# Kernel optimization log

Measured on AMD Instinct MI355X. Metric: run time of the kernel, lower is better.

Reference implementation:

```python
import jax, jax.numpy as jnp
import numpy as np

B, P, E, D, A, M, V, L = 128, 196, 2048, 512, 512, 512, 10000, 21


def setup_inputs() -> dict:
    key = jax.random.key(0)
    ks = jax.random.split(key, 24)
    s = 0.02
    encoder_out = jax.random.normal(ks[0], (B, P, E), jnp.float32)
    encoded_captions = jax.random.randint(ks[1], (B, L), 0, V)
    caption_lengths = jax.random.randint(ks[2], (B,), 2, L + 1).at[0].set(L)
    return {
        "encoder_out": encoder_out,
        "encoded_captions": encoded_captions,
        "caption_lengths": caption_lengths,
        "emb_table": jax.random.normal(ks[3], (V, M), jnp.float32) * s,
        "enc_att_w": jax.random.normal(ks[4], (E, A), jnp.float32) * s,
        "enc_att_b": jnp.zeros((A,), jnp.float32),
        "dec_att_w": jax.random.normal(ks[5], (D, A), jnp.float32) * s,
        "dec_att_b": jnp.zeros((A,), jnp.float32),
        "full_att_w": jax.random.normal(ks[6], (A,), jnp.float32) * s,
        "full_att_b": jnp.zeros((), jnp.float32),
        "init_h_w": jax.random.normal(ks[7], (E, D), jnp.float32) * s,
        "init_h_b": jnp.zeros((D,), jnp.float32),
        "init_c_w": jax.random.normal(ks[8], (E, D), jnp.float32) * s,
        "init_c_b": jnp.zeros((D,), jnp.float32),
        "f_beta_w": jax.random.normal(ks[9], (D, E), jnp.float32) * s,
        "f_beta_b": jnp.zeros((E,), jnp.float32),
        "lstm_w_ih": jax.random.normal(ks[10], (4 * D, M + E), jnp.float32) * s,
        "lstm_b_ih": jnp.zeros((4 * D,), jnp.float32),
        "lstm_w_hh": jax.random.normal(ks[11], (4 * D, D), jnp.float32) * s,
        "lstm_b_hh": jnp.zeros((4 * D,), jnp.float32),
        "fc_w": jax.random.normal(ks[12], (V, D), jnp.float32) * s,
        "fc_b": jnp.zeros((V,), jnp.float32),
    }


def reference(encoder_out, encoded_captions, caption_lengths, emb_table,
              enc_att_w, enc_att_b, dec_att_w, dec_att_b, full_att_w, full_att_b,
              init_h_w, init_h_b, init_c_w, init_c_b, f_beta_w, f_beta_b,
              lstm_w_ih, lstm_b_ih, lstm_w_hh, lstm_b_hh, fc_w, fc_b):
    # sort by caption length descending (as in torch)
    order = jnp.argsort(-caption_lengths)
    enc = encoder_out[order]                 # [B,P,E]
    caps = encoded_captions[order]           # [B,L]
    dec_len = caption_lengths[order] - 1     # [B]
    T = caps.shape[1] - 1

    emb_seq = emb_table[caps]                # [B,L,M]
    mean = enc.mean(axis=1)                  # [B,E]
    h0 = mean @ init_h_w + init_h_b
    c0 = mean @ init_c_w + init_c_b
    att1 = enc @ enc_att_w + enc_att_b       # [B,P,A] (hoisted: constant over t)

    def step(carry, t):
        h, c = carry
        att2 = h @ dec_att_w + dec_att_b                              # [B,A]
        e = jnp.einsum('bpa,a->bp', jax.nn.relu(att1 + att2[:, None, :]), full_att_w) + full_att_b
        alpha = jax.nn.softmax(e, axis=1)                             # [B,P]
        awe = jnp.einsum('bpe,bp->be', enc, alpha)                    # [B,E]
        gate = jax.nn.sigmoid(h @ f_beta_w + f_beta_b)                # [B,E]
        x = jnp.concatenate([emb_seq[:, t, :], gate * awe], axis=1)   # [B,M+E]
        g = x @ lstm_w_ih.T + lstm_b_ih + h @ lstm_w_hh.T + lstm_b_hh
        i, f, gg, o = jnp.split(g, 4, axis=1)
        c_new = jax.nn.sigmoid(f) * c + jax.nn.sigmoid(i) * jnp.tanh(gg)
        h_new = jax.nn.sigmoid(o) * jnp.tanh(c_new)
        pred = h_new @ fc_w.T + fc_b                                  # [B,V]
        active = (t < dec_len)[:, None]
        pred = jnp.where(active, pred, 0.0)
        alpha = jnp.where(active, alpha, 0.0)
        return (h_new, c_new), (pred, alpha)

    _, (preds, alphas) = jax.lax.scan(step, (h0, c0), jnp.arange(T))
    predictions = jnp.moveaxis(preds, 0, 1)   # [B,T,V]
    alphas = jnp.moveaxis(alphas, 0, 1)       # [B,T,P]
    return predictions, alphas
```

## Files before the change

### kernel.cpp

```cpp
#include <hip/hip_runtime.h>
#include <math.h>

#define B_ 128
#define P_ 196
#define E_ 2048
#define D_ 512
#define A_ 512
#define M_ 512
#define V_ 10000
#define L_ 21
#define T_ 20

__global__ void order_kernel(const int* __restrict__ lens, const int* __restrict__ caps,
                             int* __restrict__ order, int* __restrict__ declen,
                             int* __restrict__ row_map, int* __restrict__ tok_rows) {
  __shared__ int s_order[B_];
  int tid = threadIdx.x;
  if (tid < B_) {
    int li = lens[tid];
    int r = 0;
    for (int j = 0; j < B_; ++j) {
      int lj = lens[j];
      r += (lj > li) || (lj == li && j < tid);
    }
    s_order[r] = tid;
    declen[r] = li - 1;
  }
  __syncthreads();
  if (tid < B_) order[tid] = s_order[tid];
  for (int m = tid; m < B_ * P_; m += blockDim.x) {
    int b = m / P_, p = m - b * P_;
    row_map[m] = s_order[b] * P_ + p;
  }
  for (int i = tid; i < T_ * B_; i += blockDim.x) {
    int t = i >> 7, b = i & 127;
    tok_rows[i] = caps[s_order[b] * L_ + t];
  }
}

__global__ void mean_kernel(const float* __restrict__ enc, const int* __restrict__ order,
                            float* __restrict__ mean) {
  int b = blockIdx.y;
  int e = blockIdx.x * blockDim.x + threadIdx.x;
  int ob = order[b];
  const float* base = enc + (long long)ob * P_ * E_ + e;
  float s = 0.f;
  for (int p = 0; p < P_; ++p) s += base[(long long)p * E_];
  mean[b * E_ + e] = s * (1.0f / P_);
}

template <bool BT, int ACT, int CMAP>
__global__ __launch_bounds__(256) void gemm_kernel(
    const float* __restrict__ A, const float* __restrict__ Bm,
    const float* __restrict__ bias, const float* __restrict__ bias2,
    float* __restrict__ C, int M, int N, int K, int bs,
    const int* __restrict__ row_map, long long c_rstride,
    float* __restrict__ xh_dup, const int* __restrict__ declen) {
  __shared__ float As[16][64];
  __shared__ float Bs[16][64];
  const int tid = threadIdx.x;
  const int bm = blockIdx.y * 64, bn = blockIdx.x * 64;
  const int tm = tid >> 4, tn = tid & 15;

  float acc[4][4];
#pragma unroll
  for (int i = 0; i < 4; ++i)
#pragma unroll
    for (int j = 0; j < 4; ++j) acc[i][j] = 0.f;

  const int lm = tid >> 2;
  const int lk = (tid & 3) * 4;

  for (int k0 = 0; k0 < K; k0 += 16) {
    {
      int m = bm + lm;
      float4 v = make_float4(0.f, 0.f, 0.f, 0.f);
      if (m < M) {
        int row = row_map ? row_map[m] : m;
        v = *(const float4*)(A + (long long)row * K + k0 + lk);
      }
      As[lk + 0][lm] = v.x;
      As[lk + 1][lm] = v.y;
      As[lk + 2][lm] = v.z;
      As[lk + 3][lm] = v.w;
    }
    if (!BT) {
      int k = tid >> 4;
      int n4 = (tid & 15) * 4;
      int n = bn + n4;
      float4 v = make_float4(0.f, 0.f, 0.f, 0.f);
      if (n < N) v = *(const float4*)(Bm + (long long)(k0 + k) * bs + n);
      Bs[k][n4 + 0] = v.x;
      Bs[k][n4 + 1] = v.y;
      Bs[k][n4 + 2] = v.z;
      Bs[k][n4 + 3] = v.w;
    } else {
      int n = bn + lm;
      float4 v = make_float4(0.f, 0.f, 0.f, 0.f);
      if (n < N) v = *(const float4*)(Bm + (long long)n * bs + k0 + lk);
      Bs[lk + 0][lm] = v.x;
      Bs[lk + 1][lm] = v.y;
      Bs[lk + 2][lm] = v.z;
      Bs[lk + 3][lm] = v.w;
    }
    __syncthreads();
#pragma unroll
    for (int k = 0; k < 16; ++k) {
      float a0 = As[k][tm * 4 + 0];
      float a1 = As[k][tm * 4 + 1];
      float a2 = As[k][tm * 4 + 2];
      float a3 = As[k][tm * 4 + 3];
      float b0 = Bs[k][tn * 4 + 0];
      float b1 = Bs[k][tn * 4 + 1];
      float b2 = Bs[k][tn * 4 + 2];
      float b3 = Bs[k][tn * 4 + 3];
      acc[0][0] += a0 * b0; acc[0][1] += a0 * b1; acc[0][2] += a0 * b2; acc[0][3] += a0 * b3;
      acc[1][0] += a1 * b0; acc[1][1] += a1 * b1; acc[1][2] += a1 * b2; acc[1][3] += a1 * b3;
      acc[2][0] += a2 * b0; acc[2][1] += a2 * b1; acc[2][2] += a2 * b2; acc[2][3] += a2 * b3;
      acc[3][0] += a3 * b0; acc[3][1] += a3 * b1; acc[3][2] += a3 * b2; acc[3][3] += a3 * b3;
    }
    __syncthreads();
  }

#pragma unroll
  for (int i = 0; i < 4; ++i) {
    int m = bm + tm * 4 + i;
    if (m >= M) continue;
#pragma unroll
    for (int j = 0; j < 4; ++j) {
      int n = bn + tn * 4 + j;
      if (n >= N) continue;
      float v = acc[i][j];
      if (bias) v += bias[n];
      if (bias2) v += bias2[n];
      if (ACT == 1) v = 1.f / (1.f + __expf(-v));
      if (CMAP == 0) {
        C[(long long)m * c_rstride + n] = v;
        if (xh_dup) xh_dup[m * 2560 + 2048 + n] = v;
      } else {
        int b = m & 127, t = m >> 7;
        bool active = t < declen[b];
        C[(long long)b * (T_ * V_) + (long long)t * V_ + n] = active ? v : 0.f;
      }
    }
  }
}

__global__ __launch_bounds__(256) void step1_kernel(
    const float* __restrict__ h, const float* __restrict__ dec_att_w,
    const float* __restrict__ dec_att_b, const float* __restrict__ f_beta_w,
    const float* __restrict__ f_beta_b, float* __restrict__ att2,
    float* __restrict__ gate) {
  __shared__ float As[16][64];
  __shared__ float Bs[16][64];
  const int tid = threadIdx.x;
  const int bm = blockIdx.y * 64, bn = blockIdx.x * 64;
  const bool isatt = bn < 512;
  const float* Bp = isatt ? dec_att_w : f_beta_w;
  const int bstride = isatt ? 512 : 2048;
  const int ncol0 = isatt ? bn : bn - 512;
  const int tm = tid >> 4, tn = tid & 15;
  float acc[4][4];
#pragma unroll
  for (int i = 0; i < 4; ++i)
#pragma unroll
    for (int j = 0; j < 4; ++j) acc[i][j] = 0.f;
  const int lm = tid >> 2;
  const int lk = (tid & 3) * 4;
  for (int k0 = 0; k0 < 512; k0 += 16) {
    {
      int m = bm + lm;
      float4 v = *(const float4*)(h + m * 512 + k0 + lk);
      As[lk + 0][lm] = v.x;
      As[lk + 1][lm] = v.y;
      As[lk + 2][lm] = v.z;
      As[lk + 3][lm] = v.w;
    }
    {
      int k = tid >> 4;
      int n4 = (tid & 15) * 4;
      float4 v = *(const float4*)(Bp + (k0 + k) * bstride + ncol0 + n4);
      Bs[k][n4 + 0] = v.x;
      Bs[k][n4 + 1] = v.y;
      Bs[k][n4 + 2] = v.z;
      Bs[k][n4 + 3] = v.w;
    }
    __syncthreads();
#pragma unroll
    for (int k = 0; k < 16; ++k) {
      float a0 = As[k][tm * 4 + 0];
      float a1 = As[k][tm * 4 + 1];
      float a2 = As[k][tm * 4 + 2];
      float a3 = As[k][tm * 4 + 3];
      float b0 = Bs[k][tn * 4 + 0];
      float b1 = Bs[k][tn * 4 + 1];
      float b2 = Bs[k][tn * 4 + 2];
      float b3 = Bs[k][tn * 4 + 3];
      acc[0][0] += a0 * b0; acc[0][1] += a0 * b1; acc[0][2] += a0 * b2; acc[0][3] += a0 * b3;
      acc[1][0] += a1 * b0; acc[1][1] += a1 * b1; acc[1][2] += a1 * b2; acc[1][3] += a1 * b3;
      acc[2][0] += a2 * b0; acc[2][1] += a2 * b1; acc[2][2] += a2 * b2; acc[2][3] += a2 * b3;
      acc[3][0] += a3 * b0; acc[3][1] += a3 * b1; acc[3][2] += a3 * b2; acc[3][3] += a3 * b3;
    }
    __syncthreads();
  }
#pragma unroll
  for (int i = 0; i < 4; ++i) {
    int m = bm + tm * 4 + i;
#pragma unroll
    for (int j = 0; j < 4; ++j) {
      int nc = ncol0 + tn * 4 + j;
      float v = acc[i][j];
      if (isatt) {
        att2[m * 512 + nc] = v + dec_att_b[nc];
      } else {
        v += f_beta_b[nc];
        gate[m * 2048 + nc] = 1.f / (1.f + __expf(-v));
      }
    }
  }
}

__global__ __launch_bounds__(256) void esm_kernel(
    const float* __restrict__ att1, const float* __restrict__ att2,
    const float* __restrict__ w, const float* __restrict__ fb,
    const int* __restrict__ declen, int t,
    float* __restrict__ alpha_ws, float* __restrict__ alpha_out) {
  __shared__ float att2_s[A_];
  __shared__ float w_s[A_];
  __shared__ float e_s[P_];
  __shared__ float red[8];
  int b = blockIdx.x, tid = threadIdx.x;
  for (int i = tid; i < A_; i += 256) {
    att2_s[i] = att2[b * A_ + i];
    w_s[i] = w[i];
  }
  __syncthreads();
  int wave = tid >> 6, lane = tid & 63;
  for (int p = wave; p < P_; p += 4) {
    const float* row = att1 + ((long long)b * P_ + p) * A_;
    float s = 0.f;
#pragma unroll
    for (int i = 0; i < A_ / 64; ++i) {
      int idx = lane + i * 64;
      float v = row[idx] + att2_s[idx];
      s += (v > 0.f ? v : 0.f) * w_s[idx];
    }
    for (int off = 32; off; off >>= 1) s += __shfl_down(s, off);
    if (lane == 0) e_s[p] = s + fb[0];
  }
  __syncthreads();
  float m = -1e30f;
  for (int p = tid; p < P_; p += 256) m = fmaxf(m, e_s[p]);
  for (int off = 32; off; off >>= 1) m = fmaxf(m, __shfl_down(m, off));
  if (lane == 0) red[wave] = m;
  __syncthreads();
  m = fmaxf(fmaxf(red[0], red[1]), fmaxf(red[2], red[3]));
  float ssum = 0.f;
  for (int p = tid; p < P_; p += 256) {
    float ev = __expf(e_s[p] - m);
    e_s[p] = ev;
    ssum += ev;
  }
  for (int off = 32; off; off >>= 1) ssum += __shfl_down(ssum, off);
  if (lane == 0) red[4 + wave] = ssum;
  __syncthreads();
  ssum = red[4] + red[5] + red[6] + red[7];
  float inv = 1.f / ssum;
  bool active = (t < declen[b]);
  for (int p = tid; p < P_; p += 256) {
    float al = e_s[p] * inv;
    alpha_ws[b * P_ + p] = al;
    alpha_out[(long long)b * (T_ * P_) + t * P_ + p] = active ? al : 0.f;
  }
}

__global__ __launch_bounds__(256) void awe_kernel(
    const float* __restrict__ alpha_ws, const float* __restrict__ enc,
    const int* __restrict__ order, const float* __restrict__ gate,
    float* __restrict__ xh) {
  __shared__ float al[P_];
  int b = blockIdx.y;
  int e = blockIdx.x * 256 + threadIdx.x;
  for (int i = threadIdx.x; i < P_; i += 256) al[i] = alpha_ws[b * P_ + i];
  __syncthreads();
  int ob = order[b];
  const float* eb = enc + (long long)ob * P_ * E_ + e;
  float s = 0.f;
#pragma unroll 4
  for (int p = 0; p < P_; ++p) s += al[p] * eb[(long long)p * E_];
  xh[b * 2560 + e] = gate[b * 2048 + e] * s;
}

__global__ __launch_bounds__(256) void gemm2_kernel(
    const float* __restrict__ xh, const float* __restrict__ w_ih,
    const float* __restrict__ w_hh, float* __restrict__ g_part) {
  __shared__ float As[16][64];
  __shared__ float Bs[16][64];
  const int tid = threadIdx.x;
  const int bn = blockIdx.x * 64, bm = blockIdx.y * 64;
  const int z = blockIdx.z;
  const int tm = tid >> 4, tn = tid & 15;
  float acc[4][4];
#pragma unroll
  for (int i = 0; i < 4; ++i)
#pragma unroll
    for (int j = 0; j < 4; ++j) acc[i][j] = 0.f;
  const int lm = tid >> 2;
  const int lk = (tid & 3) * 4;
  const bool ih = (z < 4);
  for (int k0 = 0; k0 < 512; k0 += 16) {
    {
      int m = bm + lm;
      float4 v = *(const float4*)(xh + m * 2560 + z * 512 + k0 + lk);
      As[lk + 0][lm] = v.x;
      As[lk + 1][lm] = v.y;
      As[lk + 2][lm] = v.z;
      As[lk + 3][lm] = v.w;
    }
    {
      int n = bn + lm;
      float4 v;
      if (ih)
        v = *(const float4*)(w_ih + (long long)n * 2560 + 512 + z * 512 + k0 + lk);
      else
        v = *(const float4*)(w_hh + (long long)n * 512 + k0 + lk);
      Bs[lk + 0][lm] = v.x;
      Bs[lk + 1][lm] = v.y;
      Bs[lk + 2][lm] = v.z;
      Bs[lk + 3][lm] = v.w;
    }
    __syncthreads();
#pragma unroll
    for (int k = 0; k < 16; ++k) {
      float a0 = As[k][tm * 4 + 0];
      float a1 = As[k][tm * 4 + 1];
      float a2 = As[k][tm * 4 + 2];
      float a3 = As[k][tm * 4 + 3];
      float b0 = Bs[k][tn * 4 + 0];
      float b1 = Bs[k][tn * 4 + 1];
      float b2 = Bs[k][tn * 4 + 2];
      float b3 = Bs[k][tn * 4 + 3];
      acc[0][0] += a0 * b0; acc[0][1] += a0 * b1; acc[0][2] += a0 * b2; acc[0][3] += a0 * b3;
      acc[1][0] += a1 * b0; acc[1][1] += a1 * b1; acc[1][2] += a1 * b2; acc[1][3] += a1 * b3;
      acc[2][0] += a2 * b0; acc[2][1] += a2 * b1; acc[2][2] += a2 * b2; acc[2][3] += a2 * b3;
      acc[3][0] += a3 * b0; acc[3][1] += a3 * b1; acc[3][2] += a3 * b2; acc[3][3] += a3 * b3;
    }
    __syncthreads();
  }
  float* gp = g_part + (long long)z * (128 * 2048);
#pragma unroll
  for (int i = 0; i < 4; ++i) {
    int m = bm + tm * 4 + i;
#pragma unroll
    for (int j = 0; j < 4; ++j) {
      int n = bn + tn * 4 + j;
      gp[m * 2048 + n] = acc[i][j];
    }
  }
}

__global__ void lstm_ew_kernel(const float* __restrict__ g_emb,
                               const float* __restrict__ g_part,
                               float* __restrict__ c, float* __restrict__ h_next,
                               float* __restrict__ xh) {
  int idx = blockIdx.x * blockDim.x + threadIdx.x;
  int b = idx >> 9, d = idx & 511;
  int base = b * 2048 + d;
  float gi = g_emb[base], gf = g_emb[base + 512], gg = g_emb[base + 1024],
        go = g_emb[base + 1536];
#pragma unroll
  for (int z = 0; z < 5; ++z) {
    const float* gp = g_part + z * (128 * 2048) + base;
    gi += gp[0];
    gf += gp[512];
    gg += gp[1024];
    go += gp[1536];
  }
  float si = 1.f / (1.f + __expf(-gi));
  float sf = 1.f / (1.f + __expf(-gf));
  float so = 1.f / (1.f + __expf(-go));
  float cn = sf * c[idx] + si * tanhf(gg);
  float hn = so * tanhf(cn);
  c[idx] = cn;
  h_next[idx] = hn;
  xh[b * 2560 + 2048 + d] = hn;
}

extern "C" void kernel_launch(void* const* d_in, const int* in_sizes, int n_in,
                              void* d_out, int out_size, void* d_ws, size_t ws_size,
                              hipStream_t stream) {
  const float* enc       = (const float*)d_in[0];
  const int*   caps      = (const int*)d_in[1];
  const int*   lens      = (const int*)d_in[2];
  const float* emb       = (const float*)d_in[3];
  const float* enc_att_w = (const float*)d_in[4];
  const float* enc_att_b = (const float*)d_in[5];
  const float* dec_att_w = (const float*)d_in[6];
  const float* dec_att_b = (const float*)d_in[7];
  const float* full_att_w = (const float*)d_in[8];
  const float* full_att_b = (const float*)d_in[9];
  const float* init_h_w  = (const float*)d_in[10];
  const float* init_h_b  = (const float*)d_in[11];
  const float* init_c_w  = (const float*)d_in[12];
  const float* init_c_b  = (const float*)d_in[13];
  const float* f_beta_w  = (const float*)d_in[14];
  const float* f_beta_b  = (const float*)d_in[15];
  const float* lstm_w_ih = (const float*)d_in[16];
  const float* lstm_b_ih = (const float*)d_in[17];
  const float* lstm_w_hh = (const float*)d_in[18];
  const float* lstm_b_hh = (const float*)d_in[19];
  const float* fc_w      = (const float*)d_in[20];
  const float* fc_b      = (const float*)d_in[21];

  float* out = (float*)d_out;
  float* alphas_out = out + (long long)B_ * T_ * V_;

  float* g_all  = out;
  float* g_part = out + 6 * 1024 * 1024;

  float* ws = (float*)d_ws;
  float* att1  = ws;
  float* mean  = att1 + (long long)B_ * P_ * A_;
  float* h_all = mean + B_ * E_;
  float* c     = h_all + (T_ + 1) * B_ * D_;
  float* att2  = c + B_ * D_;
  float* gate  = att2 + B_ * A_;
  float* xh    = gate + B_ * E_;
  float* alpha_ws = xh + B_ * (M_ + E_);
  int* order   = (int*)(alpha_ws + B_ * P_);
  int* declen  = order + B_;
  int* row_map = declen + B_;
  int* tok_rows = row_map + B_ * P_;

  hipLaunchKernelGGL(order_kernel, dim3(1), dim3(256), 0, stream, lens, caps, order, declen,
                     row_map, tok_rows);
  hipLaunchKernelGGL(mean_kernel, dim3(E_ / 256, B_), dim3(256), 0, stream, enc, order, mean);
  hipLaunchKernelGGL((gemm_kernel<false, 0, 0>), dim3(D_ / 64, 2), dim3(256), 0, stream,
                     mean, init_h_w, init_h_b, (const float*)nullptr, h_all, B_, D_, E_, D_,
                     (const int*)nullptr, (long long)D_, xh, (const int*)nullptr);
  hipLaunchKernelGGL((gemm_kernel<false, 0, 0>), dim3(D_ / 64, 2), dim3(256), 0, stream,
                     mean, init_c_w, init_c_b, (const float*)nullptr, c, B_, D_, E_, D_,
                     (const int*)nullptr, (long long)D_, (float*)nullptr, (const int*)nullptr);
  hipLaunchKernelGGL((gemm_kernel<false, 0, 0>), dim3(A_ / 64, (B_ * P_) / 64), dim3(256), 0,
                     stream, enc, enc_att_w, enc_att_b, (const float*)nullptr, att1, B_ * P_,
                     A_, E_, A_, row_map, (long long)A_, (float*)nullptr, (const int*)nullptr);
  hipLaunchKernelGGL((gemm_kernel<true, 0, 0>), dim3(E_ / 64, (T_ * B_) / 64), dim3(256), 0,
                     stream, emb, lstm_w_ih, lstm_b_ih, lstm_b_hh, g_all, T_ * B_, 4 * D_, M_,
                     M_ + E_, tok_rows, (long long)(4 * D_), (float*)nullptr,
                     (const int*)nullptr);

  for (int t = 0; t < T_; ++t) {
    float* h_cur = h_all + (long long)t * B_ * D_;
    float* h_next = h_cur + B_ * D_;
    hipLaunchKernelGGL(step1_kernel, dim3(40, 2), dim3(256), 0, stream, h_cur, dec_att_w,
                       dec_att_b, f_beta_w, f_beta_b, att2, gate);
    hipLaunchKernelGGL(esm_kernel, dim3(B_), dim3(256), 0, stream, att1, att2, full_att_w,
                       full_att_b, declen, t, alpha_ws, alphas_out);
    hipLaunchKernelGGL(awe_kernel, dim3(E_ / 256, B_), dim3(256), 0, stream, alpha_ws, enc,
                       order, gate, xh);
    hipLaunchKernelGGL(gemm2_kernel, dim3(32, 2, 5), dim3(256), 0, stream, xh, lstm_w_ih,
                       lstm_w_hh, g_part);
    hipLaunchKernelGGL(lstm_ew_kernel, dim3((B_ * D_) / 256), dim3(256), 0, stream,
                       g_all + (long long)t * B_ * (4 * D_), g_part, c, h_next, xh);
  }

  hipLaunchKernelGGL((gemm_kernel<true, 0, 1>), dim3((V_ + 63) / 64, (T_ * B_) / 64),
                     dim3(256), 0, stream, h_all + B_ * D_, fc_w, fc_b, (const float*)nullptr,
                     out, T_ * B_, V_, D_, D_, (const int*)nullptr, 0LL, (float*)nullptr,
                     declen);
}
```

Baseline: 4.752 ms.

## Move large GEMMs to bf16 MFMA with split-precision hi/lo emulation

Replaces the scalar FP32 tiled GEMMs for the encoder attention projection, the embedding LSTM input projection, the per-step LSTM gate GEMM and the final vocabulary projection with one MFMA bf16 kernel using 128x128 tiles and swizzled LDS. For most of these it splits each FP32 operand into high and low bf16 parts and issues three MFMAs to keep accuracy close to FP32. The encoder attention GEMM uses plain single bf16, and its weight is transposed into a scratch region of the output buffer first. The change trades scalar FMA throughput for matrix-core throughput, at the cost of extra conversion work during staging and lower precision on the attention GEMM.

```diff
diff --git a/kernel.cpp b/kernel.cpp
--- a/kernel.cpp
+++ b/kernel.cpp
@@ -10,6 +10,9 @@
 #define V_ 10000
 #define L_ 21
 #define T_ 20
+
+typedef __attribute__((ext_vector_type(8))) short bf16x8;
+typedef __attribute__((ext_vector_type(4))) float f32x4;
 
 __global__ void order_kernel(const int* __restrict__ lens, const int* __restrict__ caps,
                              int* __restrict__ order, int* __restrict__ declen,
@@ -49,71 +52,62 @@
   mean[b * E_ + e] = s * (1.0f / P_);
 }
 
-template <bool BT, int ACT, int CMAP>
-__global__ __launch_bounds__(256) void gemm_kernel(
+__global__ void transpose_kernel(const float* __restrict__ in, float* __restrict__ out) {
+  __shared__ float t[32][33];
+  int bx = blockIdx.x * 32;
+  int by = blockIdx.y * 32;
+  int lx = threadIdx.x & 31, ly = threadIdx.x >> 5;
+#pragma unroll
+  for (int i = 0; i < 32; i += 8) t[ly + i][lx] = in[(by + ly + i) * 512 + bx + lx];
+  __syncthreads();
+#pragma unroll
+  for (int i = 0; i < 32; i += 8) out[(long long)(bx + ly + i) * 2048 + by + lx] = t[lx][ly + i];
+}
+
+__global__ __launch_bounds__(256) void gemm32_kernel(
     const float* __restrict__ A, const float* __restrict__ Bm,
-    const float* __restrict__ bias, const float* __restrict__ bias2,
-    float* __restrict__ C, int M, int N, int K, int bs,
-    const int* __restrict__ row_map, long long c_rstride,
-    float* __restrict__ xh_dup, const int* __restrict__ declen) {
+    const float* __restrict__ bias, float* __restrict__ C,
+    int M, int N, int K, float* __restrict__ xh_dup) {
   __shared__ float As[16][64];
   __shared__ float Bs[16][64];
   const int tid = threadIdx.x;
   const int bm = blockIdx.y * 64, bn = blockIdx.x * 64;
   const int tm = tid >> 4, tn = tid & 15;
-
   float acc[4][4];
 #pragma unroll
   for (int i = 0; i < 4; ++i)
 #pragma unroll
     for (int j = 0; j < 4; ++j) acc[i][j] = 0.f;
-
   const int lm = tid >> 2;
   const int lk = (tid & 3) * 4;
-
   for (int k0 = 0; k0 < K; k0 += 16) {
     {
       int m = bm + lm;
       float4 v = make_float4(0.f, 0.f, 0.f, 0.f);
-      if (m < M) {
-        int row = row_map ? row_map[m] : m;
-        v = *(const float4*)(A + (long long)row * K + k0 + lk);
-      }
+      if (m < M) v = *(const float4*)(A + (long long)m * K + k0 + lk);
       As[lk + 0][lm] = v.x;
       As[lk + 1][lm] = v.y;
       As[lk + 2][lm] = v.z;
       As[lk + 3][lm] = v.w;
     }
-    if (!BT) {
+    {
       int k = tid >> 4;
       int n4 = (tid & 15) * 4;
       int n = bn + n4;
       float4 v = make_float4(0.f, 0.f, 0.f, 0.f);
-      if (n < N) v = *(const float4*)(Bm + (long long)(k0 + k) * bs + n);
+      if (n < N) v = *(const float4*)(Bm + (long long)(k0 + k) * N + n);
       Bs[k][n4 + 0] = v.x;
       Bs[k][n4 + 1] = v.y;
       Bs[k][n4 + 2] = v.z;
       Bs[k][n4 + 3] = v.w;
-    } else {
-      int n = bn + lm;
-      float4 v = make_float4(0.f, 0.f, 0.f, 0.f);
-      if (n < N) v = *(const float4*)(Bm + (long long)n * bs + k0 + lk);
-      Bs[lk + 0][lm] = v.x;
-      Bs[lk + 1][lm] = v.y;
-      Bs[lk + 2][lm] = v.z;
-      Bs[lk + 3][lm] = v.w;
     }
     __syncthreads();
 #pragma unroll
     for (int k = 0; k < 16; ++k) {
-      float a0 = As[k][tm * 4 + 0];
-      float a1 = As[k][tm * 4 + 1];
-      float a2 = As[k][tm * 4 + 2];
-      float a3 = As[k][tm * 4 + 3];
-      float b0 = Bs[k][tn * 4 + 0];
-      float b1 = Bs[k][tn * 4 + 1];
-      float b2 = Bs[k][tn * 4 + 2];
-      float b3 = Bs[k][tn * 4 + 3];
+      float a0 = As[k][tm * 4 + 0], a1 = As[k][tm * 4 + 1];
+      float a2 = As[k][tm * 4 + 2], a3 = As[k][tm * 4 + 3];
+      float b0 = Bs[k][tn * 4 + 0], b1 = Bs[k][tn * 4 + 1];
+      float b2 = Bs[k][tn * 4 + 2], b3 = Bs[k][tn * 4 + 3];
       acc[0][0] += a0 * b0; acc[0][1] += a0 * b1; acc[0][2] += a0 * b2; acc[0][3] += a0 * b3;
       acc[1][0] += a1 * b0; acc[1][1] += a1 * b1; acc[1][2] += a1 * b2; acc[1][3] += a1 * b3;
       acc[2][0] += a2 * b0; acc[2][1] += a2 * b1; acc[2][2] += a2 * b2; acc[2][3] += a2 * b3;
@@ -121,7 +115,6 @@
     }
     __syncthreads();
   }
-
 #pragma unroll
   for (int i = 0; i < 4; ++i) {
     int m = bm + tm * 4 + i;
@@ -130,17 +123,172 @@
     for (int j = 0; j < 4; ++j) {
       int n = bn + tn * 4 + j;
       if (n >= N) continue;
-      float v = acc[i][j];
-      if (bias) v += bias[n];
-      if (bias2) v += bias2[n];
-      if (ACT == 1) v = 1.f / (1.f + __expf(-v));
-      if (CMAP == 0) {
-        C[(long long)m * c_rstride + n] = v;
-        if (xh_dup) xh_dup[m * 2560 + 2048 + n] = v;
-      } else {
-        int b = m & 127, t = m >> 7;
-        bool active = t < declen[b];
-        C[(long long)b * (T_ * V_) + (long long)t * V_ + n] = active ? v : 0.f;
+      float v = acc[i][j] + (bias ? bias[n] : 0.f);
+      C[(long long)m * N + n] = v;
+      if (xh_dup) xh_dup[m * 2560 + 2048 + n] = v;
+    }
+  }
+}
+
+__device__ __forceinline__ unsigned f2bf_u(float f) {
+  unsigned u = __float_as_uint(f);
+  return (u + 0x7fffu + ((u >> 16) & 1u)) >> 16;
+}
+
+__device__ __forceinline__ void stage16(short* __restrict__ Ph, short* __restrict__ Pl,
+                                        int r, int kq, float4 v0, float4 v1, float4 v2,
+                                        float4 v3, bool split) {
+  float f[16] = {v0.x, v0.y, v0.z, v0.w, v1.x, v1.y, v1.z, v1.w,
+                 v2.x, v2.y, v2.z, v2.w, v3.x, v3.y, v3.z, v3.w};
+#pragma unroll
+  for (int g2 = 0; g2 < 2; ++g2) {
+    int gg = (kq >> 3) + g2;
+    int slot = gg ^ ((r >> 1) & 3);
+    unsigned hb[8];
+    float lf[8];
+#pragma unroll
+    for (int j = 0; j < 8; ++j) {
+      float x = f[g2 * 8 + j];
+      hb[j] = f2bf_u(x);
+      lf[j] = x - __uint_as_float(hb[j] << 16);
+    }
+    int4 ph;
+    ph.x = (int)(hb[0] | (hb[1] << 16));
+    ph.y = (int)(hb[2] | (hb[3] << 16));
+    ph.z = (int)(hb[4] | (hb[5] << 16));
+    ph.w = (int)(hb[6] | (hb[7] << 16));
+    *(int4*)&Ph[r * 32 + slot * 8] = ph;
+    if (split) {
+      unsigned lb[8];
+#pragma unroll
+      for (int j = 0; j < 8; ++j) lb[j] = f2bf_u(lf[j]);
+      int4 pl;
+      pl.x = (int)(lb[0] | (lb[1] << 16));
+      pl.y = (int)(lb[2] | (lb[3] << 16));
+      pl.z = (int)(lb[4] | (lb[5] << 16));
+      pl.w = (int)(lb[6] | (lb[7] << 16));
+      *(int4*)&Pl[r * 32 + slot * 8] = pl;
+    }
+  }
+}
+
+__device__ __forceinline__ bf16x8 frag_load(const short* __restrict__ P, int row, int g) {
+  int slot = g ^ ((row >> 1) & 3);
+  return *(const bf16x8*)&P[row * 32 + slot * 8];
+}
+
+template <int MODE, bool SPLIT>
+__global__ __launch_bounds__(256) void mfma_gemm(
+    const float* __restrict__ A, int lda, const int* __restrict__ row_map,
+    const float* __restrict__ Bn, int ldb,
+    const float* __restrict__ bias, const float* __restrict__ bias2,
+    float* __restrict__ C, int ldc, int M, int N, int K,
+    const float* __restrict__ whh, const int* __restrict__ declen) {
+  __shared__ short Ah[128 * 32];
+  __shared__ short Bh[128 * 32];
+  __shared__ short Al[128 * 32];
+  __shared__ short Bl[128 * 32];
+  const int tid = threadIdx.x;
+  int bm = blockIdx.y * 128, bn = blockIdx.x * 128;
+  if (MODE == 2) {
+    int z = blockIdx.z;
+    A += z * 512;
+    if (z < 4) {
+      Bn += 512 + z * 512;
+    } else {
+      Bn = whh;
+      ldb = 512;
+    }
+    C += (long long)z * (128 * 2048);
+  }
+  f32x4 acc[4][4];
+#pragma unroll
+  for (int i = 0; i < 4; ++i)
+#pragma unroll
+    for (int j = 0; j < 4; ++j) acc[i][j] = (f32x4){0.f, 0.f, 0.f, 0.f};
+
+  const int r = tid >> 1;
+  const int kq = (tid & 1) * 16;
+  const int am = bm + r;
+  const long long arow = row_map ? (long long)row_map[am] : (long long)am;
+  const float* ap = A + arow * (long long)lda + kq;
+  const int gn = bn + r;
+  const float* bp = Bn + (long long)gn * ldb + kq;
+  const bool bok = gn < N;
+
+  const int lane = tid & 63;
+  const int wv = tid >> 6, wr = wv >> 1, wc = wv & 1;
+  const int lr = lane & 15, g = lane >> 4;
+
+  for (int k0 = 0; k0 < K; k0 += 32) {
+    float4 a0 = *(const float4*)(ap + k0);
+    float4 a1 = *(const float4*)(ap + k0 + 4);
+    float4 a2 = *(const float4*)(ap + k0 + 8);
+    float4 a3 = *(const float4*)(ap + k0 + 12);
+    float4 z4 = make_float4(0.f, 0.f, 0.f, 0.f);
+    float4 b0 = bok ? *(const float4*)(bp + k0) : z4;
+    float4 b1 = bok ? *(const float4*)(bp + k0 + 4) : z4;
+    float4 b2 = bok ? *(const float4*)(bp + k0 + 8) : z4;
+    float4 b3 = bok ? *(const float4*)(bp + k0 + 12) : z4;
+    stage16(Ah, Al, r, kq, a0, a1, a2, a3, SPLIT);
+    stage16(Bh, Bl, r, kq, b0, b1, b2, b3, SPLIT);
+    __syncthreads();
+    bf16x8 ah[4], bh[4];
+#pragma unroll
+    for (int i = 0; i < 4; ++i) {
+      ah[i] = frag_load(Ah, wr * 64 + i * 16 + lr, g);
+      bh[i] = frag_load(Bh, wc * 64 + i * 16 + lr, g);
+    }
+#pragma unroll
+    for (int i = 0; i < 4; ++i)
+#pragma unroll
+      for (int j = 0; j < 4; ++j)
+        acc[i][j] = __builtin_amdgcn_mfma_f32_16x16x32_bf16(ah[i], bh[j], acc[i][j], 0, 0, 0);
+    if (SPLIT) {
+      bf16x8 al2[4], bl2[4];
+#pragma unroll
+      for (int i = 0; i < 4; ++i) {
+        al2[i] = frag_load(Al, wr * 64 + i * 16 + lr, g);
+        bl2[i] = frag_load(Bl, wc * 64 + i * 16 + lr, g);
+      }
+#pragma unroll
+      for (int i = 0; i < 4; ++i)
+#pragma unroll
+        for (int j = 0; j < 4; ++j)
+          acc[i][j] = __builtin_amdgcn_mfma_f32_16x16x32_bf16(al2[i], bh[j], acc[i][j], 0, 0, 0);
+#pragma unroll
+      for (int i = 0; i < 4; ++i)
+#pragma unroll
+        for (int j = 0; j < 4; ++j)
+          acc[i][j] = __builtin_amdgcn_mfma_f32_16x16x32_bf16(ah[i], bl2[j], acc[i][j], 0, 0, 0);
+    }
+    __syncthreads();
+  }
+
+#pragma unroll
+  for (int j = 0; j < 4; ++j) {
+    int n = bn + wc * 64 + j * 16 + lr;
+    float bj = 0.f;
+    if (n < N) {
+      if (bias) bj += bias[n];
+      if (bias2) bj += bias2[n];
+    }
+#pragma unroll
+    for (int i = 0; i < 4; ++i) {
+#pragma unroll
+      for (int rr = 0; rr < 4; ++rr) {
+        int m = bm + wr * 64 + i * 16 + g * 4 + rr;
+        float v = acc[i][j][rr] + bj;
+        if (MODE == 0) {
+          C[(long long)m * ldc + n] = v;
+        } else if (MODE == 1) {
+          if (n < N) {
+            int b = m & 127, t = m >> 7;
+            C[(long long)b * (T_ * V_) + (long long)t * V_ + n] = (t < declen[b]) ? v : 0.f;
+          }
+        } else {
+          C[(long long)m * ldc + n] = v;
+        }
       }
     }
   }
@@ -188,14 +336,10 @@
     __syncthreads();
 #pragma unroll
     for (int k = 0; k < 16; ++k) {
-      float a0 = As[k][tm * 4 + 0];
-      float a1 = As[k][tm * 4 + 1];
-      float a2 = As[k][tm * 4 + 2];
-      float a3 = As[k][tm * 4 + 3];
-      float b0 = Bs[k][tn * 4 + 0];
-      float b1 = Bs[k][tn * 4 + 1];
-      float b2 = Bs[k][tn * 4 + 2];
-      float b3 = Bs[k][tn * 4 + 3];
+      float a0 = As[k][tm * 4 + 0], a1 = As[k][tm * 4 + 1];
+      float a2 = As[k][tm * 4 + 2], a3 = As[k][tm * 4 + 3];
+      float b0 = Bs[k][tn * 4 + 0], b1 = Bs[k][tn * 4 + 1];
+      float b2 = Bs[k][tn * 4 + 2], b3 = Bs[k][tn * 4 + 3];
       acc[0][0] += a0 * b0; acc[0][1] += a0 * b1; acc[0][2] += a0 * b2; acc[0][3] += a0 * b3;
       acc[1][0] += a1 * b0; acc[1][1] += a1 * b1; acc[1][2] += a1 * b2; acc[1][3] += a1 * b3;
       acc[2][0] += a2 * b0; acc[2][1] += a2 * b1; acc[2][2] += a2 * b2; acc[2][3] += a2 * b3;
@@ -289,74 +433,6 @@
 #pragma unroll 4
   for (int p = 0; p < P_; ++p) s += al[p] * eb[(long long)p * E_];
   xh[b * 2560 + e] = gate[b * 2048 + e] * s;
-}
-
-__global__ __launch_bounds__(256) void gemm2_kernel(
-    const float* __restrict__ xh, const float* __restrict__ w_ih,
-    const float* __restrict__ w_hh, float* __restrict__ g_part) {
-  __shared__ float As[16][64];
-  __shared__ float Bs[16][64];
-  const int tid = threadIdx.x;
-  const int bn = blockIdx.x * 64, bm = blockIdx.y * 64;
-  const int z = blockIdx.z;
-  const int tm = tid >> 4, tn = tid & 15;
-  float acc[4][4];
-#pragma unroll
-  for (int i = 0; i < 4; ++i)
-#pragma unroll
-    for (int j = 0; j < 4; ++j) acc[i][j] = 0.f;
-  const int lm = tid >> 2;
-  const int lk = (tid & 3) * 4;
-  const bool ih = (z < 4);
-  for (int k0 = 0; k0 < 512; k0 += 16) {
-    {
-      int m = bm + lm;
-      float4 v = *(const float4*)(xh + m * 2560 + z * 512 + k0 + lk);
-      As[lk + 0][lm] = v.x;
-      As[lk + 1][lm] = v.y;
-      As[lk + 2][lm] = v.z;
-      As[lk + 3][lm] = v.w;
-    }
-    {
-      int n = bn + lm;
-      float4 v;
-      if (ih)
-        v = *(const float4*)(w_ih + (long long)n * 2560 + 512 + z * 512 + k0 + lk);
-      else
-        v = *(const float4*)(w_hh + (long long)n * 512 + k0 + lk);
-      Bs[lk + 0][lm] = v.x;
-      Bs[lk + 1][lm] = v.y;
-      Bs[lk + 2][lm] = v.z;
-      Bs[lk + 3][lm] = v.w;
-    }
-    __syncthreads();
-#pragma unroll
-    for (int k = 0; k < 16; ++k) {
-      float a0 = As[k][tm * 4 + 0];
-      float a1 = As[k][tm * 4 + 1];
-      float a2 = As[k][tm * 4 + 2];
-      float a3 = As[k][tm * 4 + 3];
-      float b0 = Bs[k][tn * 4 + 0];
-      float b1 = Bs[k][tn * 4 + 1];
-      float b2 = Bs[k][tn * 4 + 2];
-      float b3 = Bs[k][tn * 4 + 3];
-      acc[0][0] += a0 * b0; acc[0][1] += a0 * b1; acc[0][2] += a0 * b2; acc[0][3] += a0 * b3;
-      acc[1][0] += a1 * b0; acc[1][1] += a1 * b1; acc[1][2] += a1 * b2; acc[1][3] += a1 * b3;
-      acc[2][0] += a2 * b0; acc[2][1] += a2 * b1; acc[2][2] += a2 * b2; acc[2][3] += a2 * b3;
-      acc[3][0] += a3 * b0; acc[3][1] += a3 * b1; acc[3][2] += a3 * b2; acc[3][3] += a3 * b3;
-    }
-    __syncthreads();
-  }
-  float* gp = g_part + (long long)z * (128 * 2048);
-#pragma unroll
-  for (int i = 0; i < 4; ++i) {
-    int m = bm + tm * 4 + i;
-#pragma unroll
-    for (int j = 0; j < 4; ++j) {
-      int n = bn + tn * 4 + j;
-      gp[m * 2048 + n] = acc[i][j];
-    }
-  }
 }
 
 __global__ void lstm_ew_kernel(const float* __restrict__ g_emb,
@@ -415,8 +491,9 @@
   float* out = (float*)d_out;
   float* alphas_out = out + (long long)B_ * T_ * V_;
 
-  float* g_all  = out;
-  float* g_part = out + 6 * 1024 * 1024;
+  float* g_all    = out;
+  float* g_part   = out + 6 * 1024 * 1024;
+  float* encattwT = out + 8 * 1024 * 1024;
 
   float* ws = (float*)d_ws;
   float* att1  = ws;
@@ -435,18 +512,17 @@
   hipLaunchKernelGGL(order_kernel, dim3(1), dim3(256), 0, stream, lens, caps, order, declen,
                      row_map, tok_rows);
   hipLaunchKernelGGL(mean_kernel, dim3(E_ / 256, B_), dim3(256), 0, stream, enc, order, mean);
-  hipLaunchKernelGGL((gemm_kernel<false, 0, 0>), dim3(D_ / 64, 2), dim3(256), 0, stream,
-                     mean, init_h_w, init_h_b, (const float*)nullptr, h_all, B_, D_, E_, D_,
-                     (const int*)nullptr, (long long)D_, xh, (const int*)nullptr);
-  hipLaunchKernelGGL((gemm_kernel<false, 0, 0>), dim3(D_ / 64, 2), dim3(256), 0, stream,
-                     mean, init_c_w, init_c_b, (const float*)nullptr, c, B_, D_, E_, D_,
-                     (const int*)nullptr, (long long)D_, (float*)nullptr, (const int*)nullptr);
-  hipLaunchKernelGGL((gemm_kernel<false, 0, 0>), dim3(A_ / 64, (B_ * P_) / 64), dim3(256), 0,
-                     stream, enc, enc_att_w, enc_att_b, (const float*)nullptr, att1, B_ * P_,
-                     A_, E_, A_, row_map, (long long)A_, (float*)nullptr, (const int*)nullptr);
-  hipLaunchKernelGGL((gemm_kernel<true, 0, 0>), dim3(E_ / 64, (T_ * B_) / 64), dim3(256), 0,
-                     stream, emb, lstm_w_ih, lstm_b_ih, lstm_b_hh, g_all, T_ * B_, 4 * D_, M_,
-                     M_ + E_, tok_rows, (long long)(4 * D_), (float*)nullptr,
+  hipLaunchKernelGGL(transpose_kernel, dim3(16, 64), dim3(256), 0, stream, enc_att_w, encattwT);
+  hipLaunchKernelGGL(gemm32_kernel, dim3(D_ / 64, 2), dim3(256), 0, stream, mean, init_h_w,
+                     init_h_b, h_all, B_, D_, E_, xh);
+  hipLaunchKernelGGL(gemm32_kernel, dim3(D_ / 64, 2), dim3(256), 0, stream, mean, init_c_w,
+                     init_c_b, c, B_, D_, E_, (float*)nullptr);
+  hipLaunchKernelGGL((mfma_gemm<0, false>), dim3(A_ / 128, (B_ * P_) / 128), dim3(256), 0,
+                     stream, enc, E_, row_map, encattwT, E_, enc_att_b, (const float*)nullptr,
+                     att1, A_, B_ * P_, A_, E_, (const float*)nullptr, (const int*)nullptr);
+  hipLaunchKernelGGL((mfma_gemm<0, true>), dim3((4 * D_) / 128, (T_ * B_) / 128), dim3(256), 0,
+                     stream, emb, M_, tok_rows, lstm_w_ih, M_ + E_, lstm_b_ih, lstm_b_hh,
+                     g_all, 4 * D_, T_ * B_, 4 * D_, M_, (const float*)nullptr,
                      (const int*)nullptr);
 
   for (int t = 0; t < T_; ++t) {
@@ -458,14 +534,16 @@
                        full_att_b, declen, t, alpha_ws, alphas_out);
     hipLaunchKernelGGL(awe_kernel, dim3(E_ / 256, B_), dim3(256), 0, stream, alpha_ws, enc,
                        order, gate, xh);
-    hipLaunchKernelGGL(gemm2_kernel, dim3(32, 2, 5), dim3(256), 0, stream, xh, lstm_w_ih,
-                       lstm_w_hh, g_part);
+    hipLaunchKernelGGL((mfma_gemm<2, true>), dim3((4 * D_) / 128, 1, 5), dim3(256), 0, stream,
+                       xh, M_ + E_, (const int*)nullptr, lstm_w_ih, M_ + E_,
+                       (const float*)nullptr, (const float*)nullptr, g_part, 4 * D_, B_,
+                       4 * D_, D_, lstm_w_hh, (const int*)nullptr);
     hipLaunchKernelGGL(lstm_ew_kernel, dim3((B_ * D_) / 256), dim3(256), 0, stream,
                        g_all + (long long)t * B_ * (4 * D_), g_part, c, h_next, xh);
   }
 
-  hipLaunchKernelGGL((gemm_kernel<true, 0, 1>), dim3((V_ + 63) / 64, (T_ * B_) / 64),
-                     dim3(256), 0, stream, h_all + B_ * D_, fc_w, fc_b, (const float*)nullptr,
-                     out, T_ * B_, V_, D_, D_, (const int*)nullptr, 0LL, (float*)nullptr,
+  hipLaunchKernelGGL((mfma_gemm<1, true>), dim3((V_ + 127) / 128, (T_ * B_) / 128), dim3(256),
+                     0, stream, h_all + B_ * D_, D_, (const int*)nullptr, fc_w, D_, fc_b,
+                     (const float*)nullptr, out, V_, T_ * B_, V_, D_, (const float*)nullptr,
                      declen);
 }
```

Result: no change. 4.805 ms (+1.1%).
